# Optimization experiments

Measured on AMD Instinct MI355X. Metric: run time of the kernel, lower is better.

## Reference

```python
import jax, jax.numpy as jnp
from jax import lax
import numpy as np

# ---- static config (matches init_kwargs) ----
B, H, W = 8, 32, 32
L = H * W                      # 1024 tokens
D_MODEL = 384
MAMBA_DIM = 192                # d_model * d_mamba_ratio
LOCAL_DIM = 192
D_INNER = 384                  # expand_m * MAMBA_DIM
D_STATE = 16
D_CONV = 4
DT_RANK = 12                   # ceil(MAMBA_DIM / 16)
NDIR = 4                       # h, h_flip, v, v_flip
RED = 48                       # int(D_INNER * 0.125), BiAttn reduce dim
INNER_C = 192                  # LOCAL_DIM * expand_c
K_C = 8                        # local block depthwise kernel size


def setup_inputs() -> dict:
    key = jax.random.key(0)
    ks = jax.random.split(key, 16)
    s = 0.02
    return {
        "x": jax.random.normal(ks[0], (B, L, D_MODEL), jnp.float32),
        "in_proj_w": jax.random.normal(ks[1], (2 * D_INNER, MAMBA_DIM)) * s,
        "A_log": jnp.broadcast_to(jnp.log(jnp.arange(1, D_STATE + 1, dtype=jnp.float32)), (NDIR, D_INNER, D_STATE)) + 0.0,
        "conv_w": jax.random.normal(ks[2], (NDIR, D_INNER, D_CONV)) * 0.2,
        "conv_b": jax.random.normal(ks[3], (NDIR, D_INNER)) * 0.02,
        "xproj_w": jax.random.normal(ks[4], (NDIR, DT_RANK + 2 * D_STATE, D_INNER)) * s,
        "dtproj_w": jax.random.normal(ks[5], (NDIR, D_INNER, DT_RANK)) * (DT_RANK ** -0.5),
        "dtproj_b": jax.random.normal(ks[6], (NDIR, D_INNER)) * 0.5 - 4.0,
        "Dp": jnp.ones((NDIR, D_INNER)),
        "out_proj_w": jax.random.normal(ks[7], (MAMBA_DIM, D_INNER)) * s,
        "attn_ln_g": jnp.ones((D_INNER,)),
        "attn_ln_b": jnp.zeros((D_INNER,)),
        "attn_gr_w": jax.random.normal(ks[8], (RED, D_INNER)) * s,
        "attn_gr_b": jnp.zeros((RED,)),
        "attn_cs_w": jax.random.normal(ks[9], (D_INNER, RED)) * s,
        "attn_cs_b": jnp.zeros((D_INNER,)),
        "pw1_w": jax.random.normal(ks[10], (2 * INNER_C, LOCAL_DIM)) * s,
        "pw1_b": jnp.zeros((2 * INNER_C,)),
        "dw_w": jax.random.normal(ks[11], (INNER_C, K_C)) * 0.2,
        "dw_b": jnp.zeros((INNER_C,)),
        "bn_g": jnp.ones((INNER_C,)),
        "bn_b": jnp.zeros((INNER_C,)),
        "pw2_w": jax.random.normal(ks[12], (LOCAL_DIM, INNER_C)) * s,
        "pw2_b": jnp.zeros((LOCAL_DIM,)),
    }


def _forward(x, in_proj_w, A_log, conv_w, conv_b, xproj_w, dtproj_w, dtproj_b, Dp,
             out_proj_w, attn_ln_g, attn_ln_b, attn_gr_w, attn_gr_b, attn_cs_w, attn_cs_b,
             pw1_w, pw1_b, dw_w, dw_b, bn_g, bn_b, pw2_w, pw2_b):
    mamba_in = x[:, :, :MAMBA_DIM]
    local_in = x[:, :, MAMBA_DIM:]

    # ---------- MultiMamba branch ----------
    xz = jnp.swapaxes(mamba_in @ in_proj_w.T, 1, 2)   # (B, 2*D_INNER, L)

    def to_dir(t, i):
        # reorder channel-last-token axis per scan direction
        if i == 0:
            return t
        if i == 1:
            return jnp.flip(t, -1)
        tv = t.reshape(B, -1, H, W).swapaxes(-1, -2).reshape(B, -1, L)  # column-major scan
        return tv if i == 2 else jnp.flip(tv, -1)

    def from_dir(t, i):
        if i == 0:
            return t
        if i == 1:
            return jnp.flip(t, -1)
        if i == 3:
            t = jnp.flip(t, -1)
        return t.reshape(B, -1, W, H).swapaxes(-1, -2).reshape(B, -1, L)

    def ssm_dir(xzd, i):
        # mamba_inner_fn_no_out_proj: causal dwconv -> silu -> x_proj -> selective scan -> gate
        xp, z = jnp.split(xzd, 2, axis=1)            # (B, D_INNER, L) each
        xpad = jnp.pad(xp, ((0, 0), (0, 0), (D_CONV - 1, 0)))
        u = lax.conv_general_dilated(xpad, conv_w[i][:, None, :], (1,), 'VALID',
                                     dimension_numbers=('NCH', 'OIH', 'NCH'),
                                     feature_group_count=D_INNER)
        u = jax.nn.silu(u + conv_b[i][None, :, None])
        dbl = jnp.einsum('bdl,rd->brl', u, xproj_w[i])
        dt = dbl[:, :DT_RANK]
        Bm = dbl[:, DT_RANK:DT_RANK + D_STATE]
        Cm = dbl[:, DT_RANK + D_STATE:]
        delta = jax.nn.softplus(jnp.einsum('brl,dr->bdl', dt, dtproj_w[i]) + dtproj_b[i][None, :, None])
        A = -jnp.exp(A_log[i])                        # (D_INNER, D_STATE)

        def step(h, inps):
            d_t, B_t, C_t, u_t = inps                 # (B,d),(B,n),(B,n),(B,d)
            h = jnp.exp(d_t[:, :, None] * A) * h + (d_t * u_t)[:, :, None] * B_t[:, None, :]
            return h, jnp.einsum('bdn,bn->bd', h, C_t)

        h0 = jnp.zeros((B, D_INNER, D_STATE), x.dtype)
        _, ys = lax.scan(step, h0, (delta.transpose(2, 0, 1), Bm.transpose(2, 0, 1),
                                    Cm.transpose(2, 0, 1), u.transpose(2, 0, 1)))
        y = ys.transpose(1, 2, 0) + u * Dp[i][:, None]  # (B, D_INNER, L)
        return y * jax.nn.silu(z)

    def biattn(t):                                     # (B, L, D_INNER)
        mu = t.mean(-1, keepdims=True)
        var = ((t - mu) ** 2).mean(-1, keepdims=True)
        tn = (t - mu) / jnp.sqrt(var + 1e-5) * attn_ln_g + attn_ln_b
        g = tn.mean(1, keepdims=True)                  # global pool (B,1,D_INNER)
        g = jax.nn.gelu(g @ attn_gr_w.T + attn_gr_b, approximate=False)
        c = jax.nn.sigmoid(g @ attn_cs_w.T + attn_cs_b)
        return t * c

    acc = jnp.zeros((B, L, D_INNER), x.dtype)
    for i in range(NDIR):                              # fixed small set of directions
        out_i = from_dir(ssm_dir(to_dir(xz, i), i), i)
        acc = acc + biattn(jnp.swapaxes(out_i, 1, 2))
    mamba_out = acc @ out_proj_w.T                     # (B, L, MAMBA_DIM)

    # ---------- Local conv branch ----------
    hch = jnp.einsum('blc,oc->bol', local_in, pw1_w) + pw1_b[None, :, None]
    a, gte = jnp.split(hch, 2, axis=1)
    hch = a * jax.nn.sigmoid(gte)                      # GLU, (B, INNER_C, L)
    pad_l = K_C // 2
    pad_r = K_C // 2 - (K_C + 1) % 2                   # calc_same_padding(8) -> (4, 3)
    hpad = jnp.pad(hch, ((0, 0), (0, 0), (pad_l, pad_r)))
    hch = lax.conv_general_dilated(hpad, dw_w[:, None, :], (1,), 'VALID',
                                   dimension_numbers=('NCH', 'OIH', 'NCH'),
                                   feature_group_count=INNER_C) + dw_b[None, :, None]
    mu = hch.mean((0, 2))                              # BatchNorm1d (training-mode batch stats)
    var = hch.var((0, 2))
    hch = (hch - mu[None, :, None]) / jnp.sqrt(var + 1e-5)[None, :, None] * bn_g[None, :, None] + bn_b[None, :, None]
    hch = hch * jax.nn.sigmoid(hch)                    # Swish
    local_out = jnp.einsum('bcl,oc->blo', hch, pw2_w) + pw2_b

    return jnp.concatenate([mamba_out, local_out], axis=-1)


def reference(x, in_proj_w, A_log, conv_w, conv_b, xproj_w, dtproj_w, dtproj_b, Dp,
              out_proj_w, attn_ln_g, attn_ln_b, attn_gr_w, attn_gr_b, attn_cs_w, attn_cs_b,
              pw1_w, pw1_b, dw_w, dw_b, bn_g, bn_b, pw2_w, pw2_b):
    return _forward(x, in_proj_w, A_log, conv_w, conv_b, xproj_w, dtproj_w, dtproj_b, Dp,
                    out_proj_w, attn_ln_g, attn_ln_b, attn_gr_w, attn_gr_b, attn_cs_w, attn_cs_b,
                    pw1_w, pw1_b, dw_w, dw_b, bn_g, bn_b, pw2_w, pw2_b)
```

## Files before the change

kernel.cpp:

```cpp
#include <hip/hip_runtime.h>
#include <stdint.h>


#define DEV __device__ __forceinline__

typedef __attribute__((ext_vector_type(8))) short short8;
typedef __attribute__((ext_vector_type(4))) short short4v;
typedef __attribute__((ext_vector_type(4))) float f32x4;

DEV float bf(ushort v) { union { uint32_t u; float f; } c; c.u = ((uint32_t)v) << 16; return c.f; }
DEV ushort fbf(float f) {
  union { float f; uint32_t u; } c; c.f = f;
  uint32_t u = c.u;
  return (ushort)((u + 0x7FFFu + ((u >> 16) & 1u)) >> 16);
}

#if __has_builtin(__builtin_amdgcn_exp2f)
DEV float fexp2(float x) { return __builtin_amdgcn_exp2f(x); }
#else
DEV float fexp2(float x) { return __expf(x * 0.6931471805599453f); }
#endif

template<int CTRL>
DEV float rradd(float x) {
  return x + __int_as_float(__builtin_amdgcn_update_dpp(
      0, __float_as_int(x), CTRL, 0xF, 0xF, true));
}

DEV int pmap(int i, int j) {
  if (i == 0) return j;
  if (i == 1) return 1023 - j;
  if (i == 2) return ((j & 31) << 5) | (j >> 5);
  int k = 1023 - j; return ((k & 31) << 5) | (k >> 5);
}

DEV void cvt4(const float* __restrict__ s, ushort* __restrict__ d, int blk, int tid) {
  const int idx = (blk * 256 + tid) * 4;
  float4 v = *(const float4*)(s + idx);
  d[idx] = fbf(v.x); d[idx + 1] = fbf(v.y); d[idx + 2] = fbf(v.z); d[idx + 3] = fbf(v.w);
}

__global__ __launch_bounds__(256) void prep_all(
    const float* __restrict__ x, ushort* __restrict__ xb,
    const float* __restrict__ ipw, ushort* __restrict__ ipwb,
    const float* __restrict__ opw, ushort* __restrict__ opwb,
    const float* __restrict__ pw1w, ushort* __restrict__ pw1wb,
    const float* __restrict__ pw2w, ushort* __restrict__ pw2wb,
    const float* __restrict__ xw, ushort* __restrict__ xwp)
{
  const int bx = blockIdx.x, tid = threadIdx.x;
  if (bx < 3072)      cvt4(x, xb, bx, tid);
  else if (bx < 3216) cvt4(ipw, ipwb, bx - 3072, tid);
  else if (bx < 3288) cvt4(opw, opwb, bx - 3216, tid);
  else if (bx < 3360) cvt4(pw1w, pw1wb, bx - 3288, tid);
  else if (bx < 3396) cvt4(pw2w, pw2wb, bx - 3360, tid);
  else {
    const int row = bx - 3396;
    const int i = row >> 6, nn = row & 63;
    for (int c = tid; c < 384; c += 256)
      xwp[(size_t)row * 384 + c] = (nn < 44) ? fbf(xw[((size_t)i * 44 + nn) * 384 + c]) : (ushort)0;
  }
}

template<bool BF16OUT, bool BIAS>
__global__ __launch_bounds__(256) void gemm_bt(
    const ushort* __restrict__ A, long long sAz, int lda,
    const ushort* __restrict__ Bw, long long sBz,
    const float* __restrict__ bias,
    void* __restrict__ C, long long sCz, int ldc, int coff, int K)
{
  __shared__ ushort As[64][40];
  __shared__ ushort Bs[64][40];
  A += (size_t)blockIdx.z * sAz;
  Bw += (size_t)blockIdx.z * sBz;
  const int tid = threadIdx.x;
  const int m0 = blockIdx.x * 64, n0 = blockIdx.y * 64;
  const int w = tid >> 6, lane = tid & 63, l15 = lane & 15, quad = lane >> 4;
  const int sr = tid >> 2, sc = (tid & 3) * 8;
  f32x4 acc[4] = {};
  for (int k0 = 0; k0 < K; k0 += 32) {
    __syncthreads();
    *(short8*)&As[sr][sc] = *(const short8*)(A + (size_t)(m0 + sr) * lda + k0 + sc);
    *(short8*)&Bs[sr][sc] = *(const short8*)(Bw + (size_t)(n0 + sr) * K + k0 + sc);
    __syncthreads();
    short8 av = *(short8*)&As[w * 16 + l15][quad * 8];
#pragma unroll
    for (int nt = 0; nt < 4; nt++) {
      short8 bv = *(short8*)&Bs[nt * 16 + l15][quad * 8];
      acc[nt] = __builtin_amdgcn_mfma_f32_16x16x32_bf16(av, bv, acc[nt], 0, 0, 0);
    }
  }
  float* cf = (float*)C + (size_t)blockIdx.z * sCz;
  ushort* cb = (ushort*)C + (size_t)blockIdx.z * sCz;
#pragma unroll
  for (int nt = 0; nt < 4; nt++) {
    const int col = n0 + nt * 16 + l15;
    const float bv = BIAS ? bias[col] : 0.f;
#pragma unroll
    for (int r = 0; r < 4; r++) {
      const int row = m0 + w * 16 + quad * 4 + r;
      float v = acc[nt][r] + bv;
      if (BF16OUT) cb[(size_t)row * ldc + coff + col] = fbf(v);
      else         cf[(size_t)row * ldc + coff + col] = v;
    }
  }
}

__global__ __launch_bounds__(256) void gemm_dual(
    const ushort* __restrict__ A0, int lda0, const ushort* __restrict__ B0,
    const float* __restrict__ bias0, void* __restrict__ C0, int ldc0, int coff0, int K0,
    int nt0, int bf0,
    const ushort* __restrict__ A1, int lda1, const ushort* __restrict__ B1,
    const float* __restrict__ bias1, void* __restrict__ C1, int ldc1, int coff1, int K1,
    int bf1, float* __restrict__ bnsum)
{
  __shared__ ushort As[64][40];
  __shared__ ushort Bs[64][40];
  if (blockIdx.x == 0 && blockIdx.y == 0) {
    for (int k = threadIdx.x; k < 384; k += 256) bnsum[k] = 0.f;
  }
  const ushort* A; const ushort* Bw; const float* bias; void* C;
  int lda, ldc, coff, K, bf16o, n0;
  if ((int)blockIdx.y < nt0) {
    A = A0; lda = lda0; Bw = B0; bias = bias0; C = C0; ldc = ldc0; coff = coff0; K = K0;
    bf16o = bf0; n0 = blockIdx.y * 64;
  } else {
    A = A1; lda = lda1; Bw = B1; bias = bias1; C = C1; ldc = ldc1; coff = coff1; K = K1;
    bf16o = bf1; n0 = (blockIdx.y - nt0) * 64;
  }
  const int tid = threadIdx.x;
  const int m0 = blockIdx.x * 64;
  const int w = tid >> 6, lane = tid & 63, l15 = lane & 15, quad = lane >> 4;
  const int sr = tid >> 2, sc = (tid & 3) * 8;
  f32x4 acc[4] = {};
  for (int k0 = 0; k0 < K; k0 += 32) {
    __syncthreads();
    *(short8*)&As[sr][sc] = *(const short8*)(A + (size_t)(m0 + sr) * lda + k0 + sc);
    *(short8*)&Bs[sr][sc] = *(const short8*)(Bw + (size_t)(n0 + sr) * K + k0 + sc);
    __syncthreads();
    short8 av = *(short8*)&As[w * 16 + l15][quad * 8];
#pragma unroll
    for (int nt = 0; nt < 4; nt++) {
      short8 bv = *(short8*)&Bs[nt * 16 + l15][quad * 8];
      acc[nt] = __builtin_amdgcn_mfma_f32_16x16x32_bf16(av, bv, acc[nt], 0, 0, 0);
    }
  }
#pragma unroll
  for (int nt = 0; nt < 4; nt++) {
    const int col = n0 + nt * 16 + l15;
    const float bv = bias ? bias[col] : 0.f;
#pragma unroll
    for (int r = 0; r < 4; r++) {
      const int row = m0 + w * 16 + quad * 4 + r;
      float v = acc[nt][r] + bv;
      if (bf16o) ((ushort*)C)[(size_t)row * ldc + coff + col] = fbf(v);
      else       ((float*)C)[(size_t)row * ldc + coff + col] = v;
    }
  }
}

__global__ __launch_bounds__(256) void gemm_pw2(
    const float* __restrict__ h2, const float* __restrict__ bnsum,
    const float* __restrict__ bng, const float* __restrict__ bnb,
    const ushort* __restrict__ Bw, const float* __restrict__ bias,
    float* __restrict__ C)
{
  __shared__ ushort As[64][40];
  __shared__ ushort Bs[64][40];
  __shared__ float bsc[192], bsh[192];
  const int tid = threadIdx.x;
  const int m0 = blockIdx.x * 64, n0 = blockIdx.y * 64;
  const int w = tid >> 6, lane = tid & 63, l15 = lane & 15, quad = lane >> 4;
  const int sr = tid >> 2, sc = (tid & 3) * 8;
  for (int cth = tid; cth < 192; cth += 256) {
    float m = bnsum[cth] * (1.f / 8192.f);
    float va = bnsum[192 + cth] * (1.f / 8192.f) - m * m;
    float s = bng[cth] * rsqrtf(va + 1e-5f);
    bsc[cth] = s; bsh[cth] = bnb[cth] - m * s;
  }
  f32x4 acc[4] = {};
  for (int k0 = 0; k0 < 192; k0 += 32) {
    __syncthreads();
    {
      const float* hr = h2 + (size_t)(m0 + sr) * 192 + k0 + sc;
      f32x4 a0 = *(const f32x4*)(hr);
      f32x4 a1 = *(const f32x4*)(hr + 4);
      short8 v;
#pragma unroll
      for (int k = 0; k < 8; k++) {
        const float xx = (k < 4) ? a0[k] : a1[k - 4];
        const float xn = xx * bsc[k0 + sc + k] + bsh[k0 + sc + k];
        v[k] = (short)fbf(xn / (1.f + __expf(-xn)));
      }
      *(short8*)&As[sr][sc] = v;
    }
    *(short8*)&Bs[sr][sc] = *(const short8*)(Bw + (size_t)(n0 + sr) * 192 + k0 + sc);
    __syncthreads();
    short8 av = *(short8*)&As[w * 16 + l15][quad * 8];
#pragma unroll
    for (int nt = 0; nt < 4; nt++) {
      short8 bv = *(short8*)&Bs[nt * 16 + l15][quad * 8];
      acc[nt] = __builtin_amdgcn_mfma_f32_16x16x32_bf16(av, bv, acc[nt], 0, 0, 0);
    }
  }
#pragma unroll
  for (int nt = 0; nt < 4; nt++) {
    const int col = n0 + nt * 16 + l15;
    const float bv = bias[col];
#pragma unroll
    for (int r = 0; r < 4; r++) {
      const int row = m0 + w * 16 + quad * 4 + r;
      C[(size_t)row * 384 + 192 + col] = acc[nt][r] + bv;
    }
  }
}

__global__ __launch_bounds__(256) void convdbl_kernel(
    const ushort* __restrict__ xzb, const float* __restrict__ cw,
    const float* __restrict__ cb, const ushort* __restrict__ xwp,
    ushort* __restrict__ u, float* __restrict__ dbl)
{
  __shared__ __align__(16) ushort sxz[67][392];
  __shared__ float swt[384][4];
  __shared__ float scb[384];
  const int tid = threadIdx.x;
  const int i = blockIdx.y;
  const int m0 = blockIdx.x * 64;
  const int b = m0 >> 10, j0 = m0 & 1023;

  for (int k = tid; k < 1536; k += 256) ((float*)swt)[k] = cw[(size_t)i * 1536 + k];
  for (int k = tid; k < 384; k += 256) scb[k] = cb[i * 384 + k];
  for (int g = tid; g < 67 * 96; g += 256) {
    const int rr = g / 96, c4 = (g % 96) * 4;
    const int jj = j0 - 3 + rr;
    short4v v = {};
    if (jj >= 0)
      v = *(const short4v*)(xzb + (size_t)((b << 10) + pmap(i, jj)) * 768 + c4);
    *(short4v*)&sxz[rr][c4] = v;
  }
  __syncthreads();
  {
    const int r = tid >> 2, cp = tid & 3;
    ushort* ur = u + ((size_t)((i * 8 + b) << 10) + j0 + r) * 384 + cp * 96;
#pragma unroll 4
    for (int q = 0; q < 24; q++) {
      const int c = cp * 96 + q * 4;
      const short4v x0 = *(const short4v*)&sxz[r + 0][c];
      const short4v x1 = *(const short4v*)&sxz[r + 1][c];
      const short4v x2 = *(const short4v*)&sxz[r + 2][c];
      const short4v x3 = *(const short4v*)&sxz[r + 3][c];
      short4v o;
#pragma unroll
      for (int j = 0; j < 4; j++) {
        const f32x4 wv = *(const f32x4*)&swt[c + j][0];
        float s = bf((ushort)x0[j]) * wv[0] + bf((ushort)x1[j]) * wv[1]
                + bf((ushort)x2[j]) * wv[2] + bf((ushort)x3[j]) * wv[3] + scb[c + j];
        o[j] = (short)fbf(s / (1.f + __expf(-s)));
      }
      *(short4v*)(ur + q * 4) = o;
    }
  }
  ushort (*As)[40] = (ushort(*)[40])&sxz[0][0];
  ushort (*Bs)[40] = (ushort(*)[40])(&sxz[0][0] + 2560);
  const ushort* Au = u + (size_t)i * 8192 * 384;
  const ushort* Bw = xwp + (size_t)i * 64 * 384;
  const int w = tid >> 6, lane = tid & 63, l15 = lane & 15, quad = lane >> 4;
  const int sr = tid >> 2, sc = (tid & 3) * 8;
  f32x4 acc[4] = {};
  for (int k0 = 0; k0 < 384; k0 += 32) {
    __syncthreads();
    *(short8*)&As[sr][sc] = *(const short8*)(Au + (size_t)(m0 + sr) * 384 + k0 + sc);
    *(short8*)&Bs[sr][sc] = *(const short8*)(Bw + (size_t)sr * 384 + k0 + sc);
    __syncthreads();
    short8 av = *(short8*)&As[w * 16 + l15][quad * 8];
#pragma unroll
    for (int nt = 0; nt < 4; nt++) {
      short8 bv = *(short8*)&Bs[nt * 16 + l15][quad * 8];
      acc[nt] = __builtin_amdgcn_mfma_f32_16x16x32_bf16(av, bv, acc[nt], 0, 0, 0);
    }
  }
  float* cf = dbl + (size_t)i * 8192 * 64;
#pragma unroll
  for (int nt = 0; nt < 4; nt++) {
    const int col = nt * 16 + l15;
#pragma unroll
    for (int r = 0; r < 4; r++) {
      const int row = m0 + w * 16 + quad * 4 + r;
      cf[(size_t)row * 64 + col] = acc[nt][r];
    }
  }
}

#define NCH 16
#define CJ 64
__global__ __launch_bounds__(256, 3) void scan9b_kernel(
    const ushort* __restrict__ u,
    const float*  __restrict__ dbl,
    const ushort* __restrict__ xzb,
    const float* __restrict__ alog, const float* __restrict__ dtw,
    const float* __restrict__ dtb, const float* __restrict__ Dpw,
    ushort* __restrict__ y)
{
  const int dt0 = blockIdx.x * NCH;
  const int b = blockIdx.y, i = blockIdx.z;
  const int tid = threadIdx.x;
  const int ch = tid >> 4, n = tid & 15;
  const int srow = tid >> 2, role = tid & 3;

  __shared__ float sbc[2][CJ / 2][68];
  __shared__ float sdu[2][CJ / 2][68];
  __shared__ float sy[2][CJ][20];
  __shared__ float sDp[NCH];

  float w48[4][12], dtbv4[4];
#pragma unroll
  for (int cc = 0; cc < 4; cc++) {
    const int chp = 4 * role + cc;
#pragma unroll
    for (int r = 0; r < 12; r++) w48[cc][r] = dtw[((size_t)i * 384 + dt0 + chp) * 12 + r];
    dtbv4[cc] = dtb[i * 384 + dt0 + chp];
  }
  const float L2E = 1.4426950408889634f;
  const float Al = -__expf(alog[((size_t)i * 384 + dt0 + ch) * 16 + n]) * L2E;
  if (tid < NCH) sDp[tid] = Dpw[i * 384 + dt0 + tid];

  const float selm[4] = { (n >> 2) == 0 ? 1.f : 0.f, (n >> 2) == 1 ? 1.f : 0.f,
                          (n >> 2) == 2 ? 1.f : 0.f, (n >> 2) == 3 ? 1.f : 0.f };

  const size_t rb = (size_t)(i * 8 + b) << 10;
  const ushort* ub = u + rb * 384 + dt0;
  const float* dblb = dbl + rb * 64;
  const ushort* zb = xzb + ((size_t)b << 10) * 768 + 384 + dt0;
  ushort* yb = y + rb * 384 + dt0;

  f32x4 nd0, nd1, nd2, ns0, ns1, ns2; short4v nu, nz;
  {
    const float* src = dblb + (size_t)srow * 64;
    nd0 = *(const f32x4*)(src); nd1 = *(const f32x4*)(src + 4); nd2 = *(const f32x4*)(src + 8);
    const float* seg = src + role * 12;
    ns0 = *(const f32x4*)(seg); ns1 = *(const f32x4*)(seg + 4); ns2 = *(const f32x4*)(seg + 8);
    nu = *(const short4v*)(ub + (size_t)srow * 384 + 4 * role);
    nz = *(const short4v*)(zb + (size_t)pmap(i, srow) * 768 + 4 * role);
  }

  float h = 0.f;
  f32x4 ufp = {}, zfp = {};

  for (int c = 0; c < 16; c++) {
    const int bsel = c & 1;
    f32x4 uf, zf;
#pragma unroll
    for (int k = 0; k < 4; k++) { uf[k] = bf((ushort)nu[k]); zf[k] = bf((ushort)nz[k]); }
    if (role != 0) {
      float vals[12];
#pragma unroll
      for (int k = 0; k < 4; k++) { vals[k] = ns0[k]; vals[4 + k] = ns1[k]; vals[8 + k] = ns2[k]; }
#pragma unroll
      for (int k = 0; k < 12; k++) {
        const int f = role * 12 + k;
        if (f < 44) {
          const int isC = (f >= 28) ? 1 : 0;
          const int nn = isC ? (f - 28) : (f - 12);
          sbc[bsel][srow >> 1][4 * nn + 2 * (srow & 1) + isC] = vals[k];
        }
      }
    }
    {
      float dtr[12];
#pragma unroll
      for (int k = 0; k < 4; k++) { dtr[k] = nd0[k]; dtr[4 + k] = nd1[k]; dtr[8 + k] = nd2[k]; }
#pragma unroll
      for (int cc = 0; cc < 4; cc++) {
        float s = dtbv4[cc];
#pragma unroll
        for (int r = 0; r < 12; r++) s += dtr[r] * w48[cc][r];
        const float dl = fmaxf(s, 0.f) + __logf(1.f + __expf(-fabsf(s)));
        float2 pr; pr.x = dl; pr.y = dl * uf[cc];
        *(float2*)&sdu[bsel][srow >> 1][4 * (4 * role + cc) + 2 * (srow & 1)] = pr;
      }
    }
    __syncthreads();
    if (c > 0) {
      const int lo = pmap(i, (c - 1) * CJ + srow);
      const f32x4 y4 = *(const f32x4*)&sy[bsel ^ 1][srow][role * 4];
      short4v o;
#pragma unroll
      for (int t = 0; t < 4; t++) {
        const float z = zfp[t];
        const float val = (y4[t] + ufp[t] * sDp[role * 4 + t]) * (z / (1.f + __expf(-z)));
        o[t] = (short)fbf(val);
      }
      *(short4v*)(yb + (size_t)lo * 384 + role * 4) = o;
    }
    {
      const int cn = (c < 15) ? (c + 1) : 0;
      const int rown = cn * CJ + srow;
      const float* src = dblb + (size_t)rown * 64;
      nd0 = *(const f32x4*)(src); nd1 = *(const f32x4*)(src + 4); nd2 = *(const f32x4*)(src + 8);
      const float* seg = src + role * 12;
      ns0 = *(const f32x4*)(seg); ns1 = *(const f32x4*)(seg + 4); ns2 = *(const f32x4*)(seg + 8);
      nu = *(const short4v*)(ub + (size_t)rown * 384 + 4 * role);
      nz = *(const short4v*)(zb + (size_t)pmap(i, rown) * 768 + 4 * role);
    }
    const float* sduc = &sdu[bsel][0][4 * ch];
    const float* sbcc = &sbc[bsel][0][4 * n];
#pragma unroll
    for (int q = 0; q < 4; q++) {
      f32x4 pq = {0.f, 0.f, 0.f, 0.f};
#pragma unroll
      for (int s2 = 0; s2 < 8; s2++) {
        const f32x4 duP = *(const f32x4*)(sduc + (q * 8 + s2) * 68);
        const f32x4 bcP = *(const f32x4*)(sbcc + (q * 8 + s2) * 68);
        {
          const float e = fexp2(duP[0] * Al);
          h = e * h + duP[1] * bcP[0];
          float p = h * bcP[1];
          p = rradd<0x124>(p); p = rradd<0x128>(p);
          pq[s2 >> 1] = fmaf(selm[(2 * s2) & 3], p, pq[s2 >> 1]);
        }
        {
          const float e = fexp2(duP[2] * Al);
          h = e * h + duP[3] * bcP[2];
          float p = h * bcP[3];
          p = rradd<0x124>(p); p = rradd<0x128>(p);
          pq[s2 >> 1] = fmaf(selm[(2 * s2 + 1) & 3], p, pq[s2 >> 1]);
        }
      }
#pragma unroll
      for (int j = 0; j < 4; j++) {
        float t2 = rradd<0xB1>(pq[j]);
        t2 = rradd<0x4E>(t2);
        if ((n & 3) == 0) sy[bsel][(q << 4) | (j << 2) | (n >> 2)][ch] = t2;
      }
    }
    ufp = uf; zfp = zf;
  }
  __syncthreads();
  {
    const int lo = pmap(i, 15 * CJ + srow);
    const f32x4 y4 = *(const f32x4*)&sy[1][srow][role * 4];
    short4v o;
#pragma unroll
    for (int t = 0; t < 4; t++) {
      const float z = zfp[t];
      const float val = (y4[t] + ufp[t] * sDp[role * 4 + t]) * (z / (1.f + __expf(-z)));
      o[t] = (short)fbf(val);
    }
    *(short4v*)(yb + (size_t)lo * 384 + role * 4) = o;
  }
}

__global__ __launch_bounds__(256) void lngm_kernel(const ushort* __restrict__ y,
                                                   float* __restrict__ G16)
{
  const int slab = blockIdx.x, b = blockIdx.y, i = blockIdx.z;
  const int tid = threadIdx.x;
  const int w = tid >> 6, lane = tid & 63;
  __shared__ float smu[64], srs[64];
  __shared__ ushort sy16[64][384];
  const size_t base = (size_t)i * 8192 + b * 1024 + slab * 64;
  for (int rr = 0; rr < 16; rr++) {
    const int r = w * 16 + rr;
    const ushort* yr = y + (base + r) * 384;
    const short4v v4 = *(const short4v*)(yr + 4 * lane);
    const uint32_t v2 = *(const uint32_t*)(yr + 256 + 2 * lane);
    *(short4v*)&sy16[r][4 * lane] = v4;
    *(uint32_t*)&sy16[r][256 + 2 * lane] = v2;
    float s = 0.f, ss = 0.f;
#pragma unroll
    for (int t = 0; t < 4; t++) { float v = bf((ushort)v4[t]); s += v; ss += v * v; }
    { float v = bf((ushort)(v2 & 0xffffu)); s += v; ss += v * v; }
    { float v = bf((ushort)(v2 >> 16));     s += v; ss += v * v; }
#pragma unroll
    for (int off = 1; off < 64; off <<= 1) { s += __shfl_xor(s, off, 64); ss += __shfl_xor(ss, off, 64); }
    if (lane == 0) {
      float m = s * (1.f / 384.f);
      float va = ss * (1.f / 384.f) - m * m;
      smu[r] = m;
      srs[r] = rsqrtf(va + 1e-5f);
    }
  }
  __syncthreads();
  if (tid < 192) {
    const int c0 = tid * 2;
    float s0 = 0.f, s1 = 0.f;
#pragma unroll 8
    for (int r = 0; r < 64; r++) {
      const uint32_t pv = *(const uint32_t*)&sy16[r][c0];
      const float rs = srs[r], mu = smu[r];
      s0 += (bf((ushort)(pv & 0xffffu)) - mu) * rs;
      s1 += (bf((ushort)(pv >> 16)) - mu) * rs;
    }
    float* g = G16 + ((size_t)(i * 8 + b) * 16 + slab) * 384 + c0;
    g[0] = s0; g[1] = s1;
  }
}

__global__ __launch_bounds__(64) void gate_kernel(const float* __restrict__ G16,
    const float* __restrict__ lng, const float* __restrict__ lnb,
    const float* __restrict__ grw, const float* __restrict__ grb,
    const float* __restrict__ csw, const float* __restrict__ csb, float* __restrict__ cbuf)
{
  const int b = blockIdx.x, i = blockIdx.y;
  const int ib = i * 8 + b;
  const int lane = threadIdx.x;
  __shared__ float sG[384];
  __shared__ float g48[48];
  for (int dd = lane; dd < 384; dd += 64) {
    const float* g = G16 + (size_t)ib * 16 * 384 + dd;
    float s = 0.f;
#pragma unroll
    for (int k = 0; k < 16; k++) s += g[k * 384];
    sG[dd] = s * (1.f / 1024.f) * lng[dd] + lnb[dd];
  }
  __syncthreads();
  if (lane < 48) {
    float s = grb[lane];
    for (int dd = 0; dd < 384; dd++) s += sG[dd] * grw[lane * 384 + dd];
    g48[lane] = 0.5f * s * (1.f + erff(s * 0.70710678118f));
  }
  __syncthreads();
  for (int dd = lane; dd < 384; dd += 64) {
    float s = csb[dd];
#pragma unroll
    for (int r = 0; r < 48; r++) s += g48[r] * csw[dd * 48 + r];
    cbuf[(size_t)ib * 384 + dd] = 1.f / (1.f + __expf(-s));
  }
}

__global__ __launch_bounds__(384) void accgate_kernel(const ushort* __restrict__ y,
    const float* __restrict__ cbuf, ushort* __restrict__ accb)
{
  const int t = threadIdx.x;
  const int row = blockIdx.x * 4 + (t / 96);
  const int cg = (t % 96) * 4;
  const int b = row >> 10;
  f32x4 s = {};
#pragma unroll
  for (int i = 0; i < 4; i++) {
    const short4v v = *(const short4v*)(y + ((size_t)i * 8192 + row) * 384 + cg);
    const f32x4 cv = *(const f32x4*)(cbuf + (size_t)(i * 8 + b) * 384 + cg);
#pragma unroll
    for (int k = 0; k < 4; k++) s[k] += bf((ushort)v[k]) * cv[k];
  }
  short4v o;
#pragma unroll
  for (int k = 0; k < 4; k++) o[k] = (short)fbf(s[k]);
  *(short4v*)(accb + (size_t)row * 384 + cg) = o;
}

__global__ __launch_bounds__(192) void gludwbn_kernel(const ushort* __restrict__ hchb,
    const float* __restrict__ dww, const float* __restrict__ dwb,
    float* __restrict__ h2, float* __restrict__ bnsum)
{
  const int c = threadIdx.x;
  const int lt = blockIdx.x, b = blockIdx.y;
  __shared__ float sv[23][192];
  const int l0 = lt * 16;
#pragma unroll 4
  for (int r = 0; r < 23; r++) {
    const int ls = l0 + r - 4;
    float v = 0.f;
    if (ls >= 0 && ls < 1024) {
      const size_t rr = (size_t)((b << 10) + ls) * 384;
      const float a = bf(hchb[rr + c]);
      const float g = bf(hchb[rr + 192 + c]);
      v = a / (1.f + __expf(-g));
    }
    sv[r][c] = v;
  }
  __syncthreads();
  float wk[8];
#pragma unroll
  for (int k = 0; k < 8; k++) wk[k] = dww[(c << 3) + k];
  const float bias = dwb[c];
  float sacc = 0.f, ssacc = 0.f;
  for (int q = 0; q < 16; q++) {
    float s = bias;
#pragma unroll
    for (int k = 0; k < 8; k++) s += sv[q + k][c] * wk[k];
    h2[(size_t)((b << 10) + l0 + q) * 192 + c] = s;
    sacc += s; ssacc += s * s;
  }
  atomicAdd(&bnsum[c], sacc);
  atomicAdd(&bnsum[192 + c], ssacc);
}

extern "C" void kernel_launch(void* const* d_in, const int* in_sizes, int n_in,
                              void* d_out, int out_size, void* d_ws, size_t ws_size,
                              hipStream_t stream) {
  const float* x    = (const float*)d_in[0];
  const float* ipw  = (const float*)d_in[1];
  const float* alog = (const float*)d_in[2];
  const float* cw   = (const float*)d_in[3];
  const float* cbv  = (const float*)d_in[4];
  const float* xw   = (const float*)d_in[5];
  const float* dtw  = (const float*)d_in[6];
  const float* dtb  = (const float*)d_in[7];
  const float* Dpw  = (const float*)d_in[8];
  const float* opw  = (const float*)d_in[9];
  const float* lng  = (const float*)d_in[10];
  const float* lnb  = (const float*)d_in[11];
  const float* grw  = (const float*)d_in[12];
  const float* grb  = (const float*)d_in[13];
  const float* csw  = (const float*)d_in[14];
  const float* csb  = (const float*)d_in[15];
  const float* pw1w = (const float*)d_in[16];
  const float* pw1b = (const float*)d_in[17];
  const float* dww  = (const float*)d_in[18];
  const float* dwb  = (const float*)d_in[19];
  const float* bng  = (const float*)d_in[20];
  const float* bnb  = (const float*)d_in[21];
  const float* pw2w = (const float*)d_in[22];
  const float* pw2b = (const float*)d_in[23];
  float* out = (float*)d_out;

  char* ws = (char*)d_ws;
  ushort* xb    = (ushort*)(ws + 0);
  ushort* xzb   = (ushort*)(ws + 6291456);
  ushort* u     = (ushort*)(ws + 18874368);
  float*  dbl   = (float*)(ws + 44040192);
  ushort* y     = (ushort*)(ws + 52428800);
  ushort* accb  = (ushort*)(ws + 77594624);
  float*  G16   = (float*)(ws + 83886080);
  float*  cbuf  = (float*)(ws + 84672512);
  ushort* xwp   = (ushort*)(ws + 84721664);
  ushort* ipwb  = (ushort*)(ws + 84918272);
  ushort* opwb  = (ushort*)(ws + 85213184);
  ushort* pw1wb = (ushort*)(ws + 85360640);
  ushort* pw2wb = (ushort*)(ws + 85508096);
  float*  bnsum = (float*)(ws + 85581824);
  ushort* hchb = (ushort*)(ws + 18874368);
  float*  h2   = (float*)(ws + 34603008);

  prep_all<<<dim3(3652), 256, 0, stream>>>(x, xb, ipw, ipwb, opw, opwb,
                                           pw1w, pw1wb, pw2w, pw2wb, xw, xwp);
  gemm_bt<true, false><<<dim3(128, 12, 1), 256, 0, stream>>>(
      xb, 0, 384, ipwb, 0, nullptr, xzb, 0, 768, 0, 192);
  convdbl_kernel<<<dim3(128, 4), 256, 0, stream>>>(xzb, cw, cbv, xwp, u, dbl);
  scan9b_kernel<<<dim3(24, 8, 4), 256, 0, stream>>>(u, dbl, xzb, alog, dtw, dtb, Dpw, y);
  lngm_kernel<<<dim3(16, 8, 4), 256, 0, stream>>>(y, G16);
  gate_kernel<<<dim3(8, 4), 64, 0, stream>>>(G16, lng, lnb, grw, grb, csw, csb, cbuf);
  accgate_kernel<<<dim3(2048), 384, 0, stream>>>(y, cbuf, accb);
  gemm_dual<<<dim3(128, 9), 256, 0, stream>>>(
      accb, 384, opwb, nullptr, out, 384, 0, 384, 3, 0,
      xb + 192, 384, pw1wb, pw1b, hchb, 384, 0, 192, 1, bnsum);
  gludwbn_kernel<<<dim3(64, 8), 192, 0, stream>>>(hchb, dww, dwb, h2, bnsum);
  gemm_pw2<<<dim3(128, 3), 256, 0, stream>>>(h2, bnsum, bng, bnb, pw2wb, pw2b, out);
}
```

Measured before the change: 322.3 us.

## Single-buffer scan shared memory and widen gate kernel to 384 threads

The scan kernel drops its double-buffered shared arrays and the deferred epilogue. Each chunk now runs an extra barrier and writes its outputs right after that chunk's scan. This halves shared memory, which could allow more blocks per CU, but it adds a sync per chunk and loses the overlap of the output stores with the next chunk's work. Separately, the gate kernel goes from 64 to 384 threads, with the 48-row reduction split across 8 lanes and combined by shuffles, so its serial per-thread dot products get shorter.

Measured after the change: 312.0 us. 3.2% less time.

```diff
diff --git a/kernel.cpp b/kernel.cpp
--- a/kernel.cpp
+++ b/kernel.cpp
@@ -293,7 +293,7 @@
 
 #define NCH 16
 #define CJ 64
-__global__ __launch_bounds__(256, 3) void scan9b_kernel(
+__global__ __launch_bounds__(256, 3) void scan9_kernel(
     const ushort* __restrict__ u,
     const float*  __restrict__ dbl,
     const ushort* __restrict__ xzb,
@@ -307,9 +307,9 @@
   const int ch = tid >> 4, n = tid & 15;
   const int srow = tid >> 2, role = tid & 3;
 
-  __shared__ float sbc[2][CJ / 2][68];
-  __shared__ float sdu[2][CJ / 2][68];
-  __shared__ float sy[2][CJ][20];
+  __shared__ float sbc[CJ / 2][68];
+  __shared__ float sdu[CJ / 2][68];
+  __shared__ float sy[CJ][20];
   __shared__ float sDp[NCH];
 
   float w48[4][12], dtbv4[4];
@@ -332,6 +332,8 @@
   const float* dblb = dbl + rb * 64;
   const ushort* zb = xzb + ((size_t)b << 10) * 768 + 384 + dt0;
   ushort* yb = y + rb * 384 + dt0;
+  const float* sdup = &sdu[0][4 * ch];
+  const float* sbcp = &sbc[0][4 * n];
 
   f32x4 nd0, nd1, nd2, ns0, ns1, ns2; short4v nu, nz;
   {
@@ -344,10 +346,9 @@
   }
 
   float h = 0.f;
-  f32x4 ufp = {}, zfp = {};
 
   for (int c = 0; c < 16; c++) {
-    const int bsel = c & 1;
+    const int j0 = c * CJ;
     f32x4 uf, zf;
 #pragma unroll
     for (int k = 0; k < 4; k++) { uf[k] = bf((ushort)nu[k]); zf[k] = bf((ushort)nz[k]); }
@@ -361,7 +362,7 @@
         if (f < 44) {
           const int isC = (f >= 28) ? 1 : 0;
           const int nn = isC ? (f - 28) : (f - 12);
-          sbc[bsel][srow >> 1][4 * nn + 2 * (srow & 1) + isC] = vals[k];
+          sbc[srow >> 1][4 * nn + 2 * (srow & 1) + isC] = vals[k];
         }
       }
     }
@@ -376,22 +377,10 @@
         for (int r = 0; r < 12; r++) s += dtr[r] * w48[cc][r];
         const float dl = fmaxf(s, 0.f) + __logf(1.f + __expf(-fabsf(s)));
         float2 pr; pr.x = dl; pr.y = dl * uf[cc];
-        *(float2*)&sdu[bsel][srow >> 1][4 * (4 * role + cc) + 2 * (srow & 1)] = pr;
+        *(float2*)&sdu[srow >> 1][4 * (4 * role + cc) + 2 * (srow & 1)] = pr;
       }
     }
     __syncthreads();
-    if (c > 0) {
-      const int lo = pmap(i, (c - 1) * CJ + srow);
-      const f32x4 y4 = *(const f32x4*)&sy[bsel ^ 1][srow][role * 4];
-      short4v o;
-#pragma unroll
-      for (int t = 0; t < 4; t++) {
-        const float z = zfp[t];
-        const float val = (y4[t] + ufp[t] * sDp[role * 4 + t]) * (z / (1.f + __expf(-z)));
-        o[t] = (short)fbf(val);
-      }
-      *(short4v*)(yb + (size_t)lo * 384 + role * 4) = o;
-    }
     {
       const int cn = (c < 15) ? (c + 1) : 0;
       const int rown = cn * CJ + srow;
@@ -402,15 +391,13 @@
       nu = *(const short4v*)(ub + (size_t)rown * 384 + 4 * role);
       nz = *(const short4v*)(zb + (size_t)pmap(i, rown) * 768 + 4 * role);
     }
-    const float* sduc = &sdu[bsel][0][4 * ch];
-    const float* sbcc = &sbc[bsel][0][4 * n];
 #pragma unroll
     for (int q = 0; q < 4; q++) {
       f32x4 pq = {0.f, 0.f, 0.f, 0.f};
 #pragma unroll
       for (int s2 = 0; s2 < 8; s2++) {
-        const f32x4 duP = *(const f32x4*)(sduc + (q * 8 + s2) * 68);
-        const f32x4 bcP = *(const f32x4*)(sbcc + (q * 8 + s2) * 68);
+        const f32x4 duP = *(const f32x4*)(sdup + (q * 8 + s2) * 68);
+        const f32x4 bcP = *(const f32x4*)(sbcp + (q * 8 + s2) * 68);
         {
           const float e = fexp2(duP[0] * Al);
           h = e * h + duP[1] * bcP[0];
@@ -430,23 +417,22 @@
       for (int j = 0; j < 4; j++) {
         float t2 = rradd<0xB1>(pq[j]);
         t2 = rradd<0x4E>(t2);
-        if ((n & 3) == 0) sy[bsel][(q << 4) | (j << 2) | (n >> 2)][ch] = t2;
+        if ((n & 3) == 0) sy[(q << 4) | (j << 2) | (n >> 2)][ch] = t2;
       }
     }
-    ufp = uf; zfp = zf;
-  }
-  __syncthreads();
-  {
-    const int lo = pmap(i, 15 * CJ + srow);
-    const f32x4 y4 = *(const f32x4*)&sy[1][srow][role * 4];
-    short4v o;
-#pragma unroll
-    for (int t = 0; t < 4; t++) {
-      const float z = zfp[t];
-      const float val = (y4[t] + ufp[t] * sDp[role * 4 + t]) * (z / (1.f + __expf(-z)));
-      o[t] = (short)fbf(val);
-    }
-    *(short4v*)(yb + (size_t)lo * 384 + role * 4) = o;
+    __syncthreads();
+    {
+      const int lo = pmap(i, j0 + srow);
+      const f32x4 y4 = *(const f32x4*)&sy[srow][role * 4];
+      short4v o;
+#pragma unroll
+      for (int t = 0; t < 4; t++) {
+        const float z = zf[t];
+        const float val = (y4[t] + uf[t] * sDp[role * 4 + t]) * (z / (1.f + __expf(-z)));
+        o[t] = (short)fbf(val);
+      }
+      *(short4v*)(yb + (size_t)lo * 384 + role * 4) = o;
+    }
   }
 }
 
@@ -496,35 +482,43 @@
   }
 }
 
-__global__ __launch_bounds__(64) void gate_kernel(const float* __restrict__ G16,
+__global__ __launch_bounds__(384) void gate_kernel(const float* __restrict__ G16,
     const float* __restrict__ lng, const float* __restrict__ lnb,
     const float* __restrict__ grw, const float* __restrict__ grb,
     const float* __restrict__ csw, const float* __restrict__ csb, float* __restrict__ cbuf)
 {
   const int b = blockIdx.x, i = blockIdx.y;
   const int ib = i * 8 + b;
-  const int lane = threadIdx.x;
+  const int t = threadIdx.x;
   __shared__ float sG[384];
   __shared__ float g48[48];
-  for (int dd = lane; dd < 384; dd += 64) {
-    const float* g = G16 + (size_t)ib * 16 * 384 + dd;
+  {
+    const float* g = G16 + (size_t)ib * 16 * 384 + t;
     float s = 0.f;
 #pragma unroll
     for (int k = 0; k < 16; k++) s += g[k * 384];
-    sG[dd] = s * (1.f / 1024.f) * lng[dd] + lnb[dd];
+    sG[t] = s * (1.f / 1024.f) * lng[t] + lnb[t];
   }
   __syncthreads();
-  if (lane < 48) {
-    float s = grb[lane];
-    for (int dd = 0; dd < 384; dd++) s += sG[dd] * grw[lane * 384 + dd];
-    g48[lane] = 0.5f * s * (1.f + erff(s * 0.70710678118f));
+  {
+    const int row = t >> 3, seg = t & 7;
+    const float* wr = grw + (size_t)row * 384 + seg * 48;
+    const float* gr = sG + seg * 48;
+    float s = 0.f;
+#pragma unroll
+    for (int k = 0; k < 48; k++) s += gr[k] * wr[k];
+    s += __shfl_xor(s, 1, 64); s += __shfl_xor(s, 2, 64); s += __shfl_xor(s, 4, 64);
+    if (seg == 0) {
+      s += grb[row];
+      g48[row] = 0.5f * s * (1.f + erff(s * 0.70710678118f));
+    }
   }
   __syncthreads();
-  for (int dd = lane; dd < 384; dd += 64) {
-    float s = csb[dd];
-#pragma unroll
-    for (int r = 0; r < 48; r++) s += g48[r] * csw[dd * 48 + r];
-    cbuf[(size_t)ib * 384 + dd] = 1.f / (1.f + __expf(-s));
+  {
+    float s = csb[t];
+#pragma unroll
+    for (int r = 0; r < 48; r++) s += g48[r] * csw[(size_t)t * 48 + r];
+    cbuf[(size_t)ib * 384 + t] = 1.f / (1.f + __expf(-s));
   }
 }
 
@@ -638,9 +632,9 @@
   gemm_bt<true, false><<<dim3(128, 12, 1), 256, 0, stream>>>(
       xb, 0, 384, ipwb, 0, nullptr, xzb, 0, 768, 0, 192);
   convdbl_kernel<<<dim3(128, 4), 256, 0, stream>>>(xzb, cw, cbv, xwp, u, dbl);
-  scan9b_kernel<<<dim3(24, 8, 4), 256, 0, stream>>>(u, dbl, xzb, alog, dtw, dtb, Dpw, y);
+  scan9_kernel<<<dim3(24, 8, 4), 256, 0, stream>>>(u, dbl, xzb, alog, dtw, dtb, Dpw, y);
   lngm_kernel<<<dim3(16, 8, 4), 256, 0, stream>>>(y, G16);
-  gate_kernel<<<dim3(8, 4), 64, 0, stream>>>(G16, lng, lnb, grw, grb, csw, csb, cbuf);
+  gate_kernel<<<dim3(8, 4), 384, 0, stream>>>(G16, lng, lnb, grw, grb, csw, csb, cbuf);
   accgate_kernel<<<dim3(2048), 384, 0, stream>>>(y, cbuf, accb);
   gemm_dual<<<dim3(128, 9), 256, 0, stream>>>(
       accb, 384, opwb, nullptr, out, 384, 0, 384, 3, 0,
```
